# Kernel tuning notes

Hardware: AMD Instinct MI355X
Metric: run time of the kernel (lower is better)

Reference implementation:

```python
import jax, jax.numpy as jnp
import numpy as np


def _interp_linear(c, out_len):
    """PyTorch F.interpolate(mode='linear', align_corners=False) along last axis.
    c: (d, in_len) -> (d, out_len). Half-pixel coordinate mapping."""
    in_len = c.shape[-1]
    scale = in_len / out_len
    src = (jnp.arange(out_len, dtype=jnp.float32) + 0.5) * scale - 0.5
    src = jnp.clip(src, 0.0, in_len - 1)
    lo = jnp.floor(src).astype(jnp.int32)
    hi = jnp.minimum(lo + 1, in_len - 1)
    w = (src - lo.astype(jnp.float32)).astype(c.dtype)
    return c[..., lo] * (1.0 - w) + c[..., hi] * w


def _causal_spectrum(spec, fft_size):
    """Given the real part of a causal kernel's spectrum (1, F, d) with
    F = fft_size//2+1, recover the full complex spectrum via the Hilbert
    transform (analytic-signal window in time domain)."""
    t = jnp.fft.irfft(spec, n=fft_size, axis=1)  # even real kernel (1, fft_size, d)
    w = jnp.ones((fft_size,), dtype=t.dtype)
    w = w.at[1:fft_size // 2].set(2.0)
    w = w.at[fft_size // 2 + 1:].set(0.0)
    return jnp.fft.rfft(t * w[None, :, None], axis=1)  # (1, F, d) complex


def setup_inputs() -> dict:
    key = jax.random.key(0)
    k1, k2 = jax.random.split(key)
    B, N, D, NUM_FREQS = 8, 8192, 512, 512
    x = jax.random.normal(k1, (B, N, D), dtype=jnp.float32)
    coeffs = jax.random.normal(k2, (D, NUM_FREQS), dtype=jnp.float32)
    dc = jnp.ones((D, 1), dtype=jnp.float32)
    return {"x": x, "coeffs": coeffs, "dc": dc}


def reference(x, coeffs, dc):
    n = x.shape[-2]
    fft_size = int(2 ** int(np.ceil(np.log2(2 * n))))
    # interpolate learned real frequency coefficients up to fft_size//2 bins
    pos = _interp_linear(coeffs, fft_size // 2)          # (d, fft_size//2)
    a = jnp.concatenate([dc, pos], axis=1)               # (d, fft_size//2+1)
    a = jnp.transpose(a)[None]                           # (1, F, d)
    spec = _causal_spectrum(a, fft_size)                 # (1, F, d) complex
    xf = jnp.fft.rfft(x, n=fft_size, axis=-2)            # (B, F, d)
    out = jnp.fft.irfft(xf * spec, n=fft_size, axis=-2)  # (B, fft_size, d)
    return out[..., :n, :]
```

## Files before the change

### kernel.cpp

```cpp
#include <hip/hip_runtime.h>


#define FFT_M 8192
#define SPEC_LEN 8193

constexpr float PI_F = 3.14159265358979323846f;

__device__ __forceinline__ int swz(int k) {
    return k ^ (((k >> 4) ^ (k >> 8) ^ (k >> 12)) & 15);
}

__device__ __forceinline__ int rev13(int k) {
    int d1 = k & 3, d2 = (k >> 2) & 3, d3 = (k >> 4) & 3, d4 = (k >> 6) & 1;
    int d5 = (k >> 7) & 3, d6 = (k >> 9) & 3, d7 = (k >> 11) & 3;
    return (d1 << 11) | (d2 << 9) | (d3 << 7) | (d4 << 6) | (d5 << 4) | (d6 << 2) | d7;
}

__device__ __forceinline__ float2 cmul(float2 a, float2 b) {
    return make_float2(a.x * b.x - a.y * b.y, a.x * b.y + a.y * b.x);
}

template <int L>
__device__ void r4stage(float2* s, int tid, float sign) {
    constexpr float invL = 1.0f / (float)L;
    #pragma unroll
    for (int t = 0; t < 4; ++t) {
        int j = tid + t * 512;
        int pos = j & (L - 1);
        int blk = j - pos;
        int i0 = 4 * blk + pos;
        float2 a  = s[swz(i0)];
        float2 b  = s[swz(i0 + L)];
        float2 c  = s[swz(i0 + 2 * L)];
        float2 dd = s[swz(i0 + 3 * L)];
        float th = sign * (PI_F * 0.5f) * (float)pos * invL;
        float sn, cs;
        __sincosf(th, &sn, &cs);
        float2 w1 = make_float2(cs, sn);
        float2 w2 = cmul(w1, w1);
        float2 w3 = cmul(w2, w1);
        b = cmul(b, w1); c = cmul(c, w2); dd = cmul(dd, w3);
        float2 t0 = make_float2(a.x + c.x, a.y + c.y);
        float2 t1 = make_float2(a.x - c.x, a.y - c.y);
        float2 t2 = make_float2(b.x + dd.x, b.y + dd.y);
        float2 t3 = make_float2(b.x - dd.x, b.y - dd.y);
        float2 j3 = make_float2(-sign * t3.y, sign * t3.x);
        s[swz(i0)]         = make_float2(t0.x + t2.x, t0.y + t2.y);
        s[swz(i0 + L)]     = make_float2(t1.x + j3.x, t1.y + j3.y);
        s[swz(i0 + 2 * L)] = make_float2(t0.x - t2.x, t0.y - t2.y);
        s[swz(i0 + 3 * L)] = make_float2(t1.x - j3.x, t1.y - j3.y);
    }
    __syncthreads();
}

__device__ void r2stage(float2* s, int tid, float sign) {
    #pragma unroll
    for (int t = 0; t < 8; ++t) {
        int j = tid + t * 512;
        int pos = j & 63;
        int blk = j - pos;
        int i0 = 2 * blk + pos;
        float2 a = s[swz(i0)];
        float2 b = s[swz(i0 + 64)];
        float sn, cs;
        __sincosf(sign * (PI_F / 64.0f) * (float)pos, &sn, &cs);
        float2 wb = cmul(b, make_float2(cs, sn));
        s[swz(i0)]      = make_float2(a.x + wb.x, a.y + wb.y);
        s[swz(i0 + 64)] = make_float2(a.x - wb.x, a.y - wb.y);
    }
    __syncthreads();
}

__device__ void fft8192(float2* s, int tid, float sign) {
    #pragma unroll
    for (int t = 0; t < 16; ++t) {
        int k = tid + t * 512;
        int r = rev13(k);
        if (r > k) {
            float2 a = s[swz(k)];
            float2 b = s[swz(r)];
            s[swz(k)] = b;
            s[swz(r)] = a;
        }
    }
    __syncthreads();
    r4stage<1>(s, tid, sign);
    r4stage<4>(s, tid, sign);
    r4stage<16>(s, tid, sign);
    r2stage(s, tid, sign);
    r4stage<128>(s, tid, sign);
    r4stage<512>(s, tid, sign);
    r4stage<2048>(s, tid, sign);
}

__device__ __forceinline__ float aval(const float* C, float dcv, int idx) {
    if (idx == 0) return dcv;
    int j = idx - 1;
    float src = ((float)j + 0.5f) * 0.0625f - 0.5f;
    src = fminf(fmaxf(src, 0.0f), 511.0f);
    int lo = (int)floorf(src);
    int hi = min(lo + 1, 511);
    float w = src - (float)lo;
    return C[lo] * (1.0f - w) + C[hi] * w;
}

__global__ __launch_bounds__(512) void k0_spec(const float* __restrict__ coeffs,
                                               const float* __restrict__ dc,
                                               float2* __restrict__ spec) {
    __shared__ float2 sbuf[FFT_M];
    int d = blockIdx.x;
    int tid = threadIdx.x;
    const float* C = coeffs + d * 512;
    float dcv = dc[d];
    #pragma unroll
    for (int t = 0; t < 16; ++t) {
        int k = tid + t * 512;
        float ak = aval(C, dcv, k);
        float am = aval(C, dcv, 8192 - k);
        float Ae = 0.5f * (ak + am);
        float Ao = 0.5f * (ak - am);
        float sn, cs;
        __sincosf((PI_F / 8192.0f) * (float)k, &sn, &cs);
        sbuf[swz(k)] = make_float2(Ae - Ao * sn, Ao * cs);
    }
    __syncthreads();
    fft8192(sbuf, tid, 1.0f);
    #pragma unroll
    for (int t = 0; t < 16; ++t) {
        int n = tid + t * 512;
        float2 z = sbuf[swz(n)];
        float te = z.x * (1.0f / 8192.0f);
        float to = z.y * (1.0f / 8192.0f);
        int m0 = 2 * n;
        float he = (m0 == 0) ? te : ((m0 < 8192) ? 2.0f * te : ((m0 == 8192) ? te : 0.0f));
        float ho = (m0 + 1 < 8192) ? 2.0f * to : 0.0f;
        sbuf[swz(n)] = make_float2(he, ho);
    }
    __syncthreads();
    fft8192(sbuf, tid, -1.0f);
    float2* Sd = spec + (size_t)d * SPEC_LEN;
    const float scale = 1.0f / 8192.0f;
    #pragma unroll
    for (int t = 0; t < 8; ++t) {
        int k = tid + t * 512;
        if (k == 0) {
            float2 Z0 = sbuf[swz(0)];
            Sd[0]    = make_float2((Z0.x + Z0.y) * scale, 0.0f);
            Sd[8192] = make_float2((Z0.x - Z0.y) * scale, 0.0f);
            float2 Z4 = sbuf[swz(4096)];
            Sd[4096] = make_float2(Z4.x * scale, -Z4.y * scale);
        } else {
            int km = 8192 - k;
            float2 Zk = sbuf[swz(k)];
            float2 Zm = sbuf[swz(km)];
            float2 Xe = make_float2((Zk.x + Zm.x) * 0.5f, (Zk.y - Zm.y) * 0.5f);
            float2 dz = make_float2((Zk.x - Zm.x) * 0.5f, (Zk.y + Zm.y) * 0.5f);
            float2 Xo = make_float2(dz.y, -dz.x);
            float sn, cs;
            __sincosf(-(PI_F / 8192.0f) * (float)k, &sn, &cs);
            float2 wXo = cmul(make_float2(cs, sn), Xo);
            Sd[k]  = make_float2((Xe.x + wXo.x) * scale, (Xe.y + wXo.y) * scale);
            Sd[km] = make_float2((Xe.x - wXo.x) * scale, -(Xe.y - wXo.y) * scale);
        }
    }
}

__global__ __launch_bounds__(256) void k1_pack(const float* __restrict__ x,
                                               float2* __restrict__ zin) {
    __shared__ float tile[64][33];
    int bb = blockIdx.z;
    int nt = blockIdx.x;
    int dt = blockIdx.y;
    int tx = threadIdx.x & 31, ty = threadIdx.x >> 5;
    const float* xb = x + (size_t)bb * 8192 * 512;
    int n0 = nt * 64;
    int d0 = dt * 32;
    #pragma unroll
    for (int r = 0; r < 8; ++r) {
        int row = ty + r * 8;
        tile[row][tx] = xb[(size_t)(n0 + row) * 512 + d0 + tx];
    }
    __syncthreads();
    #pragma unroll
    for (int r = 0; r < 4; ++r) {
        int dl = ty + r * 8;
        int d  = d0 + dl;
        int np = nt * 32 + tx;
        float2 v = make_float2(tile[2 * tx][dl], tile[2 * tx + 1][dl]);
        zin[((size_t)(d * 8 + bb)) * 4096 + np] = v;
    }
}

__global__ __launch_bounds__(512) void k2_conv(const float2* zin,
                                               const float2* __restrict__ spec,
                                               float2* yout) {
    __shared__ float2 sbuf[FFT_M];
    int wg = blockIdx.x;
    int d = wg >> 3;
    int tid = threadIdx.x;
    const float2* zi = zin + (size_t)wg * 4096;
    #pragma unroll
    for (int t = 0; t < 8; ++t) {
        int n = tid + t * 512;
        sbuf[swz(n)] = zi[n];
        sbuf[swz(n + 4096)] = make_float2(0.0f, 0.0f);
    }
    __syncthreads();
    fft8192(sbuf, tid, -1.0f);
    const float2* S = spec + (size_t)d * SPEC_LEN;
    #pragma unroll
    for (int t = 0; t < 8; ++t) {
        int k = tid + t * 512;
        if (k == 0) {
            float2 Z0 = sbuf[swz(0)];
            float X0 = Z0.x + Z0.y;
            float XM = Z0.x - Z0.y;
            float2 S0 = S[0], SM = S[8192];
            float2 Y0 = make_float2(X0 * S0.x, X0 * S0.y);
            float2 YM = make_float2(XM * SM.x, XM * SM.y);
            float2 Ye = make_float2((Y0.x + YM.x) * 0.5f, (Y0.y - YM.y) * 0.5f);
            float2 Yo = make_float2((Y0.x - YM.x) * 0.5f, (Y0.y + YM.y) * 0.5f);
            sbuf[swz(0)] = make_float2(Ye.x - Yo.y, Ye.y + Yo.x);
            float2 Z4 = sbuf[swz(4096)];
            float2 Y4 = cmul(make_float2(Z4.x, -Z4.y), S[4096]);
            sbuf[swz(4096)] = make_float2(Y4.x, -Y4.y);
        } else {
            int km = 8192 - k;
            float2 Zk = sbuf[swz(k)];
            float2 Zm = sbuf[swz(km)];
            float2 Xe = make_float2((Zk.x + Zm.x) * 0.5f, (Zk.y - Zm.y) * 0.5f);
            float2 dz = make_float2((Zk.x - Zm.x) * 0.5f, (Zk.y + Zm.y) * 0.5f);
            float2 Xo = make_float2(dz.y, -dz.x);
            float sn, cs;
            __sincosf(-(PI_F / 8192.0f) * (float)k, &sn, &cs);
            float2 w = make_float2(cs, sn);
            float2 wXo = cmul(w, Xo);
            float2 Xk = make_float2(Xe.x + wXo.x, Xe.y + wXo.y);
            float2 Xm = make_float2(Xe.x - wXo.x, -(Xe.y - wXo.y));
            float2 Yk = cmul(Xk, S[k]);
            float2 Ym = cmul(Xm, S[km]);
            float2 Ye = make_float2((Yk.x + Ym.x) * 0.5f, (Yk.y - Ym.y) * 0.5f);
            float2 dy = make_float2((Yk.x - Ym.x) * 0.5f, (Yk.y + Ym.y) * 0.5f);
            float2 Yo = cmul(make_float2(cs, -sn), dy);
            sbuf[swz(k)]  = make_float2(Ye.x - Yo.y, Ye.y + Yo.x);
            sbuf[swz(km)] = make_float2(Ye.x + Yo.y, Yo.x - Ye.y);
        }
    }
    __syncthreads();
    fft8192(sbuf, tid, 1.0f);
    float2* yo = yout + (size_t)wg * 4096;
    #pragma unroll
    for (int t = 0; t < 8; ++t) {
        int n = tid + t * 512;
        yo[n] = sbuf[swz(n)];
    }
}

__global__ __launch_bounds__(256) void k3_unpack(const float2* __restrict__ yout,
                                                 float* __restrict__ out) {
    __shared__ float2 tile[32][33];
    int bb = blockIdx.z, nt = blockIdx.x, dt = blockIdx.y;
    int tx = threadIdx.x & 31, ty = threadIdx.x >> 5;
    int d0 = dt * 32, np0 = nt * 32;
    #pragma unroll
    for (int r = 0; r < 4; ++r) {
        int dl = ty + r * 8;
        tile[dl][tx] = yout[((size_t)((d0 + dl) * 8 + bb)) * 4096 + np0 + tx];
    }
    __syncthreads();
    float* ob = out + (size_t)bb * 8192 * 512;
    #pragma unroll
    for (int r = 0; r < 4; ++r) {
        int nl = ty + r * 8;
        int n  = np0 + nl;
        float2 v = tile[tx][nl];
        ob[(size_t)(2 * n) * 512 + d0 + tx]     = v.x;
        ob[(size_t)(2 * n + 1) * 512 + d0 + tx] = v.y;
    }
}

extern "C" void kernel_launch(void* const* d_in, const int* in_sizes, int n_in,
                              void* d_out, int out_size, void* d_ws, size_t ws_size,
                              hipStream_t stream) {
    const float* x      = (const float*)d_in[0];
    const float* coeffs = (const float*)d_in[1];
    const float* dc     = (const float*)d_in[2];
    float* out = (float*)d_out;

    float2* spec = (float2*)d_ws;
    float2* zbuf = (float2*)((char*)d_ws + (size_t)512 * SPEC_LEN * sizeof(float2));

    k0_spec<<<512, 512, 0, stream>>>(coeffs, dc, spec);
    k1_pack<<<dim3(128, 16, 8), 256, 0, stream>>>(x, zbuf);
    k2_conv<<<4096, 512, 0, stream>>>(zbuf, spec, zbuf);
    k3_unpack<<<dim3(128, 16, 8), 256, 0, stream>>>(zbuf, out);
}
```

Measured before the change: 593.3 us.

## Use DIF/DIT FFT pairs without bit reversal, precomputed twiddles, fused pack and spec

```diff
diff --git a/kernel.cpp b/kernel.cpp
--- a/kernel.cpp
+++ b/kernel.cpp
@@ -3,11 +3,18 @@
 
 #define FFT_M 8192
 #define SPEC_LEN 8193
-
 constexpr float PI_F = 3.14159265358979323846f;
 
+__device__ float2 g_tw[8188];
+__device__ float2 g_wu[4096];
+#define TW_R2 8124
+
+template <int L> __device__ constexpr int twbase() {
+    return L == 4 ? 0 : L == 16 ? 12 : L == 128 ? 60 : L == 512 ? 444 : 1980;
+}
+
 __device__ __forceinline__ int swz(int k) {
-    return k ^ (((k >> 4) ^ (k >> 8) ^ (k >> 12)) & 15);
+    return k ^ (((k >> 4) ^ (k >> 8)) & 15);
 }
 
 __device__ __forceinline__ int rev13(int k) {
@@ -20,31 +27,28 @@
     return make_float2(a.x * b.x - a.y * b.y, a.x * b.y + a.y * b.x);
 }
 
-template <int L>
-__device__ void r4stage(float2* s, int tid, float sign) {
-    constexpr float invL = 1.0f / (float)L;
+template <int L, int SGN>
+__device__ void r4dit(float2* s, int tid) {
     #pragma unroll
     for (int t = 0; t < 4; ++t) {
         int j = tid + t * 512;
         int pos = j & (L - 1);
-        int blk = j - pos;
-        int i0 = 4 * blk + pos;
-        float2 a  = s[swz(i0)];
-        float2 b  = s[swz(i0 + L)];
-        float2 c  = s[swz(i0 + 2 * L)];
-        float2 dd = s[swz(i0 + 3 * L)];
-        float th = sign * (PI_F * 0.5f) * (float)pos * invL;
-        float sn, cs;
-        __sincosf(th, &sn, &cs);
-        float2 w1 = make_float2(cs, sn);
-        float2 w2 = cmul(w1, w1);
-        float2 w3 = cmul(w2, w1);
-        b = cmul(b, w1); c = cmul(c, w2); dd = cmul(dd, w3);
+        int i0 = 4 * (j - pos) + pos;
+        float2 a = s[swz(i0)];
+        float2 b = s[swz(i0 + L)];
+        float2 c = s[swz(i0 + 2 * L)];
+        float2 d = s[swz(i0 + 3 * L)];
+        if constexpr (L > 1) {
+            constexpr int B = twbase<L>();
+            float2 w1 = g_tw[B + pos], w2 = g_tw[B + L + pos], w3 = g_tw[B + 2 * L + pos];
+            if constexpr (SGN > 0) { w1.y = -w1.y; w2.y = -w2.y; w3.y = -w3.y; }
+            b = cmul(b, w1); c = cmul(c, w2); d = cmul(d, w3);
+        }
         float2 t0 = make_float2(a.x + c.x, a.y + c.y);
         float2 t1 = make_float2(a.x - c.x, a.y - c.y);
-        float2 t2 = make_float2(b.x + dd.x, b.y + dd.y);
-        float2 t3 = make_float2(b.x - dd.x, b.y - dd.y);
-        float2 j3 = make_float2(-sign * t3.y, sign * t3.x);
+        float2 t2 = make_float2(b.x + d.x, b.y + d.y);
+        float2 t3 = make_float2(b.x - d.x, b.y - d.y);
+        float2 j3 = (SGN < 0) ? make_float2(t3.y, -t3.x) : make_float2(-t3.y, t3.x);
         s[swz(i0)]         = make_float2(t0.x + t2.x, t0.y + t2.y);
         s[swz(i0 + L)]     = make_float2(t1.x + j3.x, t1.y + j3.y);
         s[swz(i0 + 2 * L)] = make_float2(t0.x - t2.x, t0.y - t2.y);
@@ -53,44 +57,112 @@
     __syncthreads();
 }
 
-__device__ void r2stage(float2* s, int tid, float sign) {
+template <int L, int SGN>
+__device__ void r4dif(float2* s, int tid) {
+    #pragma unroll
+    for (int t = 0; t < 4; ++t) {
+        int j = tid + t * 512;
+        int pos = j & (L - 1);
+        int i0 = 4 * (j - pos) + pos;
+        float2 a = s[swz(i0)];
+        float2 b = s[swz(i0 + L)];
+        float2 c = s[swz(i0 + 2 * L)];
+        float2 d = s[swz(i0 + 3 * L)];
+        float2 t0 = make_float2(a.x + c.x, a.y + c.y);
+        float2 t1 = make_float2(a.x - c.x, a.y - c.y);
+        float2 t2 = make_float2(b.x + d.x, b.y + d.y);
+        float2 t3 = make_float2(b.x - d.x, b.y - d.y);
+        float2 j3 = (SGN < 0) ? make_float2(t3.y, -t3.x) : make_float2(-t3.y, t3.x);
+        float2 u0 = make_float2(t0.x + t2.x, t0.y + t2.y);
+        float2 u1 = make_float2(t1.x + j3.x, t1.y + j3.y);
+        float2 u2 = make_float2(t0.x - t2.x, t0.y - t2.y);
+        float2 u3 = make_float2(t1.x - j3.x, t1.y - j3.y);
+        if constexpr (L > 1) {
+            constexpr int B = twbase<L>();
+            float2 w1 = g_tw[B + pos], w2 = g_tw[B + L + pos], w3 = g_tw[B + 2 * L + pos];
+            if constexpr (SGN > 0) { w1.y = -w1.y; w2.y = -w2.y; w3.y = -w3.y; }
+            u1 = cmul(u1, w1); u2 = cmul(u2, w2); u3 = cmul(u3, w3);
+        }
+        s[swz(i0)]         = u0;
+        s[swz(i0 + L)]     = u1;
+        s[swz(i0 + 2 * L)] = u2;
+        s[swz(i0 + 3 * L)] = u3;
+    }
+    __syncthreads();
+}
+
+template <int SGN>
+__device__ void r2dit(float2* s, int tid) {
     #pragma unroll
     for (int t = 0; t < 8; ++t) {
         int j = tid + t * 512;
         int pos = j & 63;
-        int blk = j - pos;
-        int i0 = 2 * blk + pos;
+        int i0 = 2 * (j - pos) + pos;
         float2 a = s[swz(i0)];
         float2 b = s[swz(i0 + 64)];
-        float sn, cs;
-        __sincosf(sign * (PI_F / 64.0f) * (float)pos, &sn, &cs);
-        float2 wb = cmul(b, make_float2(cs, sn));
+        float2 w = g_tw[TW_R2 + pos];
+        if constexpr (SGN > 0) w.y = -w.y;
+        float2 wb = cmul(b, w);
         s[swz(i0)]      = make_float2(a.x + wb.x, a.y + wb.y);
         s[swz(i0 + 64)] = make_float2(a.x - wb.x, a.y - wb.y);
     }
     __syncthreads();
 }
 
-__device__ void fft8192(float2* s, int tid, float sign) {
-    #pragma unroll
-    for (int t = 0; t < 16; ++t) {
-        int k = tid + t * 512;
-        int r = rev13(k);
-        if (r > k) {
-            float2 a = s[swz(k)];
-            float2 b = s[swz(r)];
-            s[swz(k)] = b;
-            s[swz(r)] = a;
-        }
-    }
-    __syncthreads();
-    r4stage<1>(s, tid, sign);
-    r4stage<4>(s, tid, sign);
-    r4stage<16>(s, tid, sign);
-    r2stage(s, tid, sign);
-    r4stage<128>(s, tid, sign);
-    r4stage<512>(s, tid, sign);
-    r4stage<2048>(s, tid, sign);
+template <int SGN>
+__device__ void r2dif(float2* s, int tid) {
+    #pragma unroll
+    for (int t = 0; t < 8; ++t) {
+        int j = tid + t * 512;
+        int pos = j & 63;
+        int i0 = 2 * (j - pos) + pos;
+        float2 a = s[swz(i0)];
+        float2 b = s[swz(i0 + 64)];
+        float2 w = g_tw[TW_R2 + pos];
+        if constexpr (SGN > 0) w.y = -w.y;
+        float2 dd = make_float2(a.x - b.x, a.y - b.y);
+        s[swz(i0)]      = make_float2(a.x + b.x, a.y + b.y);
+        s[swz(i0 + 64)] = cmul(dd, w);
+    }
+    __syncthreads();
+}
+
+template <int SGN> __device__ void fft_dif_full(float2* s, int tid) {
+    r4dif<2048, SGN>(s, tid); r4dif<512, SGN>(s, tid); r4dif<128, SGN>(s, tid);
+    r2dif<SGN>(s, tid);
+    r4dif<16, SGN>(s, tid); r4dif<4, SGN>(s, tid); r4dif<1, SGN>(s, tid);
+}
+template <int SGN> __device__ void fft_dit_full(float2* s, int tid) {
+    r4dit<1, SGN>(s, tid); r4dit<4, SGN>(s, tid); r4dit<16, SGN>(s, tid);
+    r2dit<SGN>(s, tid);
+    r4dit<128, SGN>(s, tid); r4dit<512, SGN>(s, tid); r4dit<2048, SGN>(s, tid);
+}
+
+__global__ __launch_bounds__(512) void k_tw() {
+    int gid = blockIdx.x * 512 + threadIdx.x;
+    for (int idx = gid; idx < 8188 + 4096; idx += gridDim.x * 512) {
+        if (idx < 8124) {
+            int L, B;
+            if (idx < 12)        { L = 4;    B = 0; }
+            else if (idx < 60)   { L = 16;   B = 12; }
+            else if (idx < 444)  { L = 128;  B = 60; }
+            else if (idx < 1980) { L = 512;  B = 444; }
+            else                 { L = 2048; B = 1980; }
+            int q = idx - B;
+            int m = q / L + 1;
+            int pos = q - (m - 1) * L;
+            float ang = -2.0f * PI_F * (float)(m * pos) / (4.0f * (float)L);
+            g_tw[idx] = make_float2(cosf(ang), sinf(ang));
+        } else if (idx < 8188) {
+            int pos = idx - 8124;
+            float ang = -2.0f * PI_F * (float)pos / 128.0f;
+            g_tw[idx] = make_float2(cosf(ang), sinf(ang));
+        } else {
+            int k = idx - 8188;
+            float ang = -PI_F * (float)k / 8192.0f;
+            g_wu[k] = make_float2(cosf(ang), sinf(ang));
+        }
+    }
 }
 
 __device__ __forceinline__ float aval(const float* C, float dcv, int idx) {
@@ -104,136 +176,141 @@
     return C[lo] * (1.0f - w) + C[hi] * w;
 }
 
-__global__ __launch_bounds__(512) void k0_spec(const float* __restrict__ coeffs,
-                                               const float* __restrict__ dc,
-                                               float2* __restrict__ spec) {
+__global__ __launch_bounds__(512) void k01(const float* __restrict__ x,
+                                           const float* __restrict__ coeffs,
+                                           const float* __restrict__ dc,
+                                           float2* __restrict__ spec,
+                                           float2* __restrict__ zin) {
     __shared__ float2 sbuf[FFT_M];
-    int d = blockIdx.x;
     int tid = threadIdx.x;
-    const float* C = coeffs + d * 512;
-    float dcv = dc[d];
-    #pragma unroll
-    for (int t = 0; t < 16; ++t) {
-        int k = tid + t * 512;
-        float ak = aval(C, dcv, k);
-        float am = aval(C, dcv, 8192 - k);
-        float Ae = 0.5f * (ak + am);
-        float Ao = 0.5f * (ak - am);
-        float sn, cs;
-        __sincosf((PI_F / 8192.0f) * (float)k, &sn, &cs);
-        sbuf[swz(k)] = make_float2(Ae - Ao * sn, Ao * cs);
-    }
-    __syncthreads();
-    fft8192(sbuf, tid, 1.0f);
-    #pragma unroll
-    for (int t = 0; t < 16; ++t) {
-        int n = tid + t * 512;
-        float2 z = sbuf[swz(n)];
-        float te = z.x * (1.0f / 8192.0f);
-        float to = z.y * (1.0f / 8192.0f);
-        int m0 = 2 * n;
-        float he = (m0 == 0) ? te : ((m0 < 8192) ? 2.0f * te : ((m0 == 8192) ? te : 0.0f));
-        float ho = (m0 + 1 < 8192) ? 2.0f * to : 0.0f;
-        sbuf[swz(n)] = make_float2(he, ho);
-    }
-    __syncthreads();
-    fft8192(sbuf, tid, -1.0f);
-    float2* Sd = spec + (size_t)d * SPEC_LEN;
-    const float scale = 1.0f / 8192.0f;
+    if (blockIdx.x < 512) {
+        int d = blockIdx.x;
+        const float* C = coeffs + d * 512;
+        float dcv = dc[d];
+        #pragma unroll
+        for (int t = 0; t < 16; ++t) {
+            int k = tid + t * 512;
+            float ak = aval(C, dcv, k);
+            float am = aval(C, dcv, 8192 - k);
+            float Ae = 0.5f * (ak + am);
+            float Ao = 0.5f * (ak - am);
+            float sn, cs;
+            __sincosf((PI_F / 8192.0f) * (float)k, &sn, &cs);
+            sbuf[swz(rev13(k))] = make_float2(Ae - Ao * sn, Ao * cs);
+        }
+        __syncthreads();
+        fft_dit_full<1>(sbuf, tid);
+        #pragma unroll
+        for (int t = 0; t < 16; ++t) {
+            int n = tid + t * 512;
+            float2 z = sbuf[swz(n)];
+            float te = z.x * (1.0f / 8192.0f);
+            float to = z.y * (1.0f / 8192.0f);
+            int m0 = 2 * n;
+            float he = (m0 == 0) ? te : ((m0 < 8192) ? 2.0f * te : ((m0 == 8192) ? te : 0.0f));
+            float ho = (m0 + 1 < 8192) ? 2.0f * to : 0.0f;
+            sbuf[swz(n)] = make_float2(he, ho);
+        }
+        __syncthreads();
+        fft_dif_full<-1>(sbuf, tid);
+        float2* Sd = spec + (size_t)d * SPEC_LEN;
+        const float scale = 1.0f / 8192.0f;
+        #pragma unroll
+        for (int t = 0; t < 8; ++t) {
+            int k = tid + t * 512;
+            if (k == 0) {
+                float2 Z0 = sbuf[0];
+                Sd[0]    = make_float2((Z0.x + Z0.y) * scale, 0.0f);
+                Sd[8192] = make_float2((Z0.x - Z0.y) * scale, 0.0f);
+                float2 Z4 = sbuf[swz(rev13(4096))];
+                Sd[4096] = make_float2(Z4.x * scale, -Z4.y * scale);
+            } else {
+                int km = 8192 - k;
+                float2 Zk = sbuf[swz(rev13(k))];
+                float2 Zm = sbuf[swz(rev13(km))];
+                float2 Xe = make_float2((Zk.x + Zm.x) * 0.5f, (Zk.y - Zm.y) * 0.5f);
+                float2 dz = make_float2((Zk.x - Zm.x) * 0.5f, (Zk.y + Zm.y) * 0.5f);
+                float2 Xo = make_float2(dz.y, -dz.x);
+                float2 w = g_wu[k];
+                float2 wXo = cmul(w, Xo);
+                Sd[k]  = make_float2((Xe.x + wXo.x) * scale, (Xe.y + wXo.y) * scale);
+                Sd[km] = make_float2((Xe.x - wXo.x) * scale, -(Xe.y - wXo.y) * scale);
+            }
+        }
+    } else {
+        int bid = blockIdx.x - 512;
+        int nt = bid & 127, dt = (bid >> 7) & 15, bb = bid >> 11;
+        float* tile = (float*)sbuf;
+        int tx = tid & 31, ty = tid >> 5;
+        const float* xb = x + (size_t)bb * 8192 * 512;
+        int n0 = nt * 64, d0 = dt * 32;
+        #pragma unroll
+        for (int r = 0; r < 4; ++r) {
+            int row = ty + r * 16;
+            tile[row * 33 + tx] = xb[(size_t)(n0 + row) * 512 + d0 + tx];
+        }
+        __syncthreads();
+        #pragma unroll
+        for (int r = 0; r < 2; ++r) {
+            int dl = ty + r * 16;
+            int d  = d0 + dl;
+            int np = nt * 32 + tx;
+            float2 v = make_float2(tile[(2 * tx) * 33 + dl], tile[(2 * tx + 1) * 33 + dl]);
+            zin[((size_t)(d * 8 + bb)) * 4096 + np] = v;
+        }
+    }
+}
+
+__global__ __launch_bounds__(512) void k2_conv(const float2* __restrict__ zin,
+                                               const float2* __restrict__ spec,
+                                               float2* __restrict__ yout) {
+    __shared__ float2 sbuf[FFT_M];
+    int wg = blockIdx.x, d = wg >> 3, tid = threadIdx.x;
+    const float2* zi = zin + (size_t)wg * 4096;
+    #pragma unroll
+    for (int t = 0; t < 4; ++t) {
+        int pos = tid + t * 512;
+        float2 a = zi[pos];
+        float2 b = zi[pos + 2048];
+        constexpr int B = twbase<2048>();
+        float2 w1 = g_tw[B + pos], w2 = g_tw[B + 2048 + pos], w3 = g_tw[B + 4096 + pos];
+        float2 u1 = make_float2(a.x + b.y, a.y - b.x);
+        float2 u2 = make_float2(a.x - b.x, a.y - b.y);
+        float2 u3 = make_float2(a.x - b.y, a.y + b.x);
+        sbuf[swz(pos)]        = make_float2(a.x + b.x, a.y + b.y);
+        sbuf[swz(pos + 2048)] = cmul(u1, w1);
+        sbuf[swz(pos + 4096)] = cmul(u2, w2);
+        sbuf[swz(pos + 6144)] = cmul(u3, w3);
+    }
+    __syncthreads();
+    r4dif<512, -1>(sbuf, tid); r4dif<128, -1>(sbuf, tid);
+    r2dif<-1>(sbuf, tid);
+    r4dif<16, -1>(sbuf, tid); r4dif<4, -1>(sbuf, tid); r4dif<1, -1>(sbuf, tid);
+    const float2* S = spec + (size_t)d * SPEC_LEN;
     #pragma unroll
     for (int t = 0; t < 8; ++t) {
         int k = tid + t * 512;
         if (k == 0) {
-            float2 Z0 = sbuf[swz(0)];
-            Sd[0]    = make_float2((Z0.x + Z0.y) * scale, 0.0f);
-            Sd[8192] = make_float2((Z0.x - Z0.y) * scale, 0.0f);
-            float2 Z4 = sbuf[swz(4096)];
-            Sd[4096] = make_float2(Z4.x * scale, -Z4.y * scale);
-        } else {
-            int km = 8192 - k;
-            float2 Zk = sbuf[swz(k)];
-            float2 Zm = sbuf[swz(km)];
-            float2 Xe = make_float2((Zk.x + Zm.x) * 0.5f, (Zk.y - Zm.y) * 0.5f);
-            float2 dz = make_float2((Zk.x - Zm.x) * 0.5f, (Zk.y + Zm.y) * 0.5f);
-            float2 Xo = make_float2(dz.y, -dz.x);
-            float sn, cs;
-            __sincosf(-(PI_F / 8192.0f) * (float)k, &sn, &cs);
-            float2 wXo = cmul(make_float2(cs, sn), Xo);
-            Sd[k]  = make_float2((Xe.x + wXo.x) * scale, (Xe.y + wXo.y) * scale);
-            Sd[km] = make_float2((Xe.x - wXo.x) * scale, -(Xe.y - wXo.y) * scale);
-        }
-    }
-}
-
-__global__ __launch_bounds__(256) void k1_pack(const float* __restrict__ x,
-                                               float2* __restrict__ zin) {
-    __shared__ float tile[64][33];
-    int bb = blockIdx.z;
-    int nt = blockIdx.x;
-    int dt = blockIdx.y;
-    int tx = threadIdx.x & 31, ty = threadIdx.x >> 5;
-    const float* xb = x + (size_t)bb * 8192 * 512;
-    int n0 = nt * 64;
-    int d0 = dt * 32;
-    #pragma unroll
-    for (int r = 0; r < 8; ++r) {
-        int row = ty + r * 8;
-        tile[row][tx] = xb[(size_t)(n0 + row) * 512 + d0 + tx];
-    }
-    __syncthreads();
-    #pragma unroll
-    for (int r = 0; r < 4; ++r) {
-        int dl = ty + r * 8;
-        int d  = d0 + dl;
-        int np = nt * 32 + tx;
-        float2 v = make_float2(tile[2 * tx][dl], tile[2 * tx + 1][dl]);
-        zin[((size_t)(d * 8 + bb)) * 4096 + np] = v;
-    }
-}
-
-__global__ __launch_bounds__(512) void k2_conv(const float2* zin,
-                                               const float2* __restrict__ spec,
-                                               float2* yout) {
-    __shared__ float2 sbuf[FFT_M];
-    int wg = blockIdx.x;
-    int d = wg >> 3;
-    int tid = threadIdx.x;
-    const float2* zi = zin + (size_t)wg * 4096;
-    #pragma unroll
-    for (int t = 0; t < 8; ++t) {
-        int n = tid + t * 512;
-        sbuf[swz(n)] = zi[n];
-        sbuf[swz(n + 4096)] = make_float2(0.0f, 0.0f);
-    }
-    __syncthreads();
-    fft8192(sbuf, tid, -1.0f);
-    const float2* S = spec + (size_t)d * SPEC_LEN;
-    #pragma unroll
-    for (int t = 0; t < 8; ++t) {
-        int k = tid + t * 512;
-        if (k == 0) {
-            float2 Z0 = sbuf[swz(0)];
-            float X0 = Z0.x + Z0.y;
-            float XM = Z0.x - Z0.y;
+            float2 Z0 = sbuf[0];
+            float X0 = Z0.x + Z0.y, XM = Z0.x - Z0.y;
             float2 S0 = S[0], SM = S[8192];
             float2 Y0 = make_float2(X0 * S0.x, X0 * S0.y);
             float2 YM = make_float2(XM * SM.x, XM * SM.y);
             float2 Ye = make_float2((Y0.x + YM.x) * 0.5f, (Y0.y - YM.y) * 0.5f);
             float2 Yo = make_float2((Y0.x - YM.x) * 0.5f, (Y0.y + YM.y) * 0.5f);
-            sbuf[swz(0)] = make_float2(Ye.x - Yo.y, Ye.y + Yo.x);
-            float2 Z4 = sbuf[swz(4096)];
+            sbuf[0] = make_float2(Ye.x - Yo.y, Ye.y + Yo.x);
+            int p4 = swz(rev13(4096));
+            float2 Z4 = sbuf[p4];
             float2 Y4 = cmul(make_float2(Z4.x, -Z4.y), S[4096]);
-            sbuf[swz(4096)] = make_float2(Y4.x, -Y4.y);
+            sbuf[p4] = make_float2(Y4.x, -Y4.y);
         } else {
             int km = 8192 - k;
-            float2 Zk = sbuf[swz(k)];
-            float2 Zm = sbuf[swz(km)];
+            int p1 = swz(rev13(k)), p2 = swz(rev13(km));
+            float2 Zk = sbuf[p1], Zm = sbuf[p2];
             float2 Xe = make_float2((Zk.x + Zm.x) * 0.5f, (Zk.y - Zm.y) * 0.5f);
             float2 dz = make_float2((Zk.x - Zm.x) * 0.5f, (Zk.y + Zm.y) * 0.5f);
             float2 Xo = make_float2(dz.y, -dz.x);
-            float sn, cs;
-            __sincosf(-(PI_F / 8192.0f) * (float)k, &sn, &cs);
-            float2 w = make_float2(cs, sn);
+            float2 w = g_wu[k];
             float2 wXo = cmul(w, Xo);
             float2 Xk = make_float2(Xe.x + wXo.x, Xe.y + wXo.y);
             float2 Xm = make_float2(Xe.x - wXo.x, -(Xe.y - wXo.y));
@@ -241,18 +318,34 @@
             float2 Ym = cmul(Xm, S[km]);
             float2 Ye = make_float2((Yk.x + Ym.x) * 0.5f, (Yk.y - Ym.y) * 0.5f);
             float2 dy = make_float2((Yk.x - Ym.x) * 0.5f, (Yk.y + Ym.y) * 0.5f);
-            float2 Yo = cmul(make_float2(cs, -sn), dy);
-            sbuf[swz(k)]  = make_float2(Ye.x - Yo.y, Ye.y + Yo.x);
-            sbuf[swz(km)] = make_float2(Ye.x + Yo.y, Yo.x - Ye.y);
-        }
-    }
-    __syncthreads();
-    fft8192(sbuf, tid, 1.0f);
+            float2 Yo = cmul(make_float2(w.x, -w.y), dy);
+            sbuf[p1] = make_float2(Ye.x - Yo.y, Ye.y + Yo.x);
+            sbuf[p2] = make_float2(Ye.x + Yo.y, Yo.x - Ye.y);
+        }
+    }
+    __syncthreads();
+    r4dit<1, 1>(sbuf, tid); r4dit<4, 1>(sbuf, tid); r4dit<16, 1>(sbuf, tid);
+    r2dit<1>(sbuf, tid);
+    r4dit<128, 1>(sbuf, tid); r4dit<512, 1>(sbuf, tid);
     float2* yo = yout + (size_t)wg * 4096;
     #pragma unroll
-    for (int t = 0; t < 8; ++t) {
-        int n = tid + t * 512;
-        yo[n] = sbuf[swz(n)];
+    for (int t = 0; t < 4; ++t) {
+        int pos = tid + t * 512;
+        float2 a  = sbuf[swz(pos)];
+        float2 b  = sbuf[swz(pos + 2048)];
+        float2 c  = sbuf[swz(pos + 4096)];
+        float2 dd = sbuf[swz(pos + 6144)];
+        constexpr int B = twbase<2048>();
+        float2 w1 = g_tw[B + pos], w2 = g_tw[B + 2048 + pos], w3 = g_tw[B + 4096 + pos];
+        w1.y = -w1.y; w2.y = -w2.y; w3.y = -w3.y;
+        b = cmul(b, w1); c = cmul(c, w2); dd = cmul(dd, w3);
+        float2 t0 = make_float2(a.x + c.x, a.y + c.y);
+        float2 t1 = make_float2(a.x - c.x, a.y - c.y);
+        float2 t2 = make_float2(b.x + dd.x, b.y + dd.y);
+        float2 t3 = make_float2(b.x - dd.x, b.y - dd.y);
+        float2 j3 = make_float2(-t3.y, t3.x);
+        yo[pos]        = make_float2(t0.x + t2.x, t0.y + t2.y);
+        yo[pos + 2048] = make_float2(t1.x + j3.x, t1.y + j3.y);
     }
 }
 
@@ -290,8 +383,8 @@
     float2* spec = (float2*)d_ws;
     float2* zbuf = (float2*)((char*)d_ws + (size_t)512 * SPEC_LEN * sizeof(float2));
 
-    k0_spec<<<512, 512, 0, stream>>>(coeffs, dc, spec);
-    k1_pack<<<dim3(128, 16, 8), 256, 0, stream>>>(x, zbuf);
+    k_tw<<<24, 512, 0, stream>>>();
+    k01<<<512 + 16384, 512, 0, stream>>>(x, coeffs, dc, spec, zbuf);
     k2_conv<<<4096, 512, 0, stream>>>(zbuf, spec, zbuf);
     k3_unpack<<<dim3(128, 16, 8), 256, 0, stream>>>(zbuf, out);
 }
```

Result: slower. 637.1 us (+7.4%).
